# Kernel optimization log

Measured on AMD Instinct MI355X. Metric: run time of the kernel, lower is better.

Reference implementation:

```python
import jax, jax.numpy as jnp
import numpy as np

jax.config.update("jax_enable_x64", True)

MANT_SCALE = 8388608.0  # 2**23


def _decode_fp32_bits(bits):
    """[..., 32] {0,1} pulses (MSB-first IEEE-754 float32) -> float64 value."""
    f64 = jnp.float64
    sign = 1.0 - 2.0 * bits[..., 0].astype(f64)
    e = jnp.einsum('...j,j->...', bits[..., 1:9].astype(f64),
                   jnp.exp2(jnp.arange(7, -1, -1, dtype=f64)))
    frac = jnp.einsum('...j,j->...', bits[..., 9:32].astype(f64),
                      jnp.exp2(-jnp.arange(1, 24, dtype=f64)))
    normal = sign * jnp.exp2(e - 127.0) * (1.0 + frac)
    subnorm = sign * jnp.exp2(-126.0) * frac
    return jnp.where(e > 0, normal, subnorm)


def _encode_fp32_bits(y):
    """float64 value already on the fp32 grid -> [..., 32] {0,1} pulses (MSB-first)."""
    f64 = jnp.float64
    sbit = (y < 0).astype(f64)
    a = jnp.abs(y)
    e = jnp.clip(jnp.floor(jnp.log2(jnp.where(a > 0, a, 1.0))), -126.0, 127.0)
    eb = jnp.where(a > 0, e + 127.0, 0.0)          # biased exponent, 0 for zero/subnormal
    frac = jnp.where(eb > 0, a * jnp.exp2(-e) - 1.0, a * jnp.exp2(126.0))
    mant = frac * MANT_SCALE                        # exact integer for fp32-grid y
    ebits = jnp.mod(jnp.floor(eb[..., None] * jnp.exp2(-jnp.arange(7, -1, -1, dtype=f64))), 2.0)
    mbits = jnp.mod(jnp.floor(mant[..., None] * jnp.exp2(-jnp.arange(22, -1, -1, dtype=f64))), 2.0)
    bits = jnp.concatenate([sbit[..., None], ebits, mbits], axis=-1)
    return jnp.where((a > 0)[..., None], bits, 0.0).astype(jnp.float32)


def setup_inputs() -> dict:
    rng = np.random.default_rng(0)
    vals = (rng.standard_normal((1, 2048, 1024)) * 2.0).astype(np.float32)
    words = vals.view(np.uint32)
    shifts = np.arange(31, -1, -1, dtype=np.uint32)
    bits = ((words[..., None] >> shifts) & np.uint32(1)).astype(np.float32)
    return {"x": jnp.asarray(bits)}


def reference(x):
    # GELU(x) ~= x * sigmoid(1.702 * x), all intermediates in fp64 (as the
    # gate-level pipeline does), final result rounded once to fp32 bits.
    xv = _decode_fp32_bits(x)
    y64 = xv * jax.nn.sigmoid(1.702 * xv)
    y32 = y64.astype(jnp.float32).astype(jnp.float64)  # FP64 -> FP32 rounding
    return _encode_fp32_bits(y32)
```

## Files before the change

### kernel.cpp

```cpp
#include <hip/hip_runtime.h>
#include <math.h>

__global__ __launch_bounds__(256) void spike_gelu_kernel(
    const uint4* __restrict__ in, uint4* __restrict__ out, int n_vals) {
#pragma clang fp contract(off)
  const double LN2 = 0x1.62e42fefa39efp-1;

  __shared__ double Wdec[8], Vdec[23], Lm[23];
  int tid = threadIdx.x;
  if (tid < 8)       Wdec[tid]      = exp((double)(7 - tid) * LN2);
  else if (tid < 31) Vdec[tid - 8]  = exp((double)(7 - tid) * LN2);
  else if (tid < 54) Lm[tid - 31]   = exp((double)(31 - tid) * LN2);
  __syncthreads();

  int v = blockIdx.x * blockDim.x + tid;
  if (v >= n_vals) return;

  const uint4* p = in + (size_t)v * 8;
  uint32_t w = 0;
#pragma unroll
  for (int j = 0; j < 8; ++j) {
    uint4 b = p[j];
    w = (w << 4) | (((b.x >> 23) & 1u) << 3) | (((b.y >> 23) & 1u) << 2) |
        (((b.z >> 23) & 1u) << 1) | ((b.w >> 23) & 1u);
  }

  double sign = (w >> 31) ? -1.0 : 1.0;
  double e_c = 0.0;
#pragma unroll
  for (int j = 0; j < 8; ++j)
    if ((w >> (30 - j)) & 1u) e_c = e_c + Wdec[j];
  double frac_d = 0.0;
#pragma unroll
  for (int j = 0; j < 23; ++j)
    if ((w >> (22 - j)) & 1u) frac_d = frac_d + Vdec[j];

  double x;
  if (e_c > 0.0) {
    double E1 = exp((e_c - 127.0) * LN2);
    x = (sign * E1) * (1.0 + frac_d);
  } else {
    x = (sign * exp(-126.0 * LN2)) * frac_d;
  }

  double t = 1.702 * x;
  double s = 1.0 / (1.0 + exp(-t));
  double y = x * s;
  float yf = (float)y;
  double yd = (double)yf;

  double a = fabs(yd);
  uint32_t ob = 0;
  if (a > 0.0) {
    if (yd < 0.0) ob |= 0x80000000u;
    double e0 = floor(log(a) / LN2);
    e0 = fmin(fmax(e0, -126.0), 127.0);
    double eb = e0 + 127.0;
    double p2 = exp(-e0 * LN2);
    double m1 = a * p2;
    double frac_e = m1 - 1.0;
    double mant = frac_e * 8388608.0;
#pragma unroll
    for (int sc = 7; sc >= 0; --sc) {
      double f = floor(eb * Lm[sc]);
      double md = f - 2.0 * floor(0.5 * f);
      ob |= ((uint32_t)md) << (23 + sc);
    }
#pragma unroll
    for (int sc = 22; sc >= 0; --sc) {
      double f = floor(mant * Lm[sc]);
      double md = f - 2.0 * floor(0.5 * f);
      ob |= ((uint32_t)md) << sc;
    }
  }

  uint4* q = out + (size_t)v * 8;
#pragma unroll
  for (int j = 0; j < 8; ++j) {
    int base = 31 - 4 * j;
    uint4 o;
    o.x = ((ob >> base) & 1u) * 0x3F800000u;
    o.y = ((ob >> (base - 1)) & 1u) * 0x3F800000u;
    o.z = ((ob >> (base - 2)) & 1u) * 0x3F800000u;
    o.w = ((ob >> (base - 3)) & 1u) * 0x3F800000u;
    q[j] = o;
  }
}

extern "C" void kernel_launch(void* const* d_in, const int* in_sizes, int n_in,
                              void* d_out, int out_size, void* d_ws, size_t ws_size,
                              hipStream_t stream) {
  int n_vals = in_sizes[0] / 32;
  const int block = 256;
  int grid = (n_vals + block - 1) / block;
  spike_gelu_kernel<<<grid, block, 0, stream>>>(
      (const uint4*)d_in[0], (uint4*)d_out, n_vals);
}
```

Baseline: 484.8 us.

## Coalesce bit-pulse loads and stores via wave shuffles and LDS staging

Each thread now loads consecutive 16-byte chunks so global reads are fully coalesced across the wave, assembling 32-bit words from nibbles with xor shuffles and staging them in shared memory. After computing, results are written back to shared memory and expanded into coalesced uint4 stores. This replaces the per-thread strided 128-byte access pattern, at the cost of two block barriers and extra LDS traffic.

```diff
diff --git a/kernel.cpp b/kernel.cpp
--- a/kernel.cpp
+++ b/kernel.cpp
@@ -7,83 +7,103 @@
   const double LN2 = 0x1.62e42fefa39efp-1;
 
   __shared__ double Wdec[8], Vdec[23], Lm[23];
-  int tid = threadIdx.x;
+  __shared__ uint32_t lds_w[256];
+
+  const int tid = threadIdx.x;
   if (tid < 8)       Wdec[tid]      = exp((double)(7 - tid) * LN2);
   else if (tid < 31) Vdec[tid - 8]  = exp((double)(7 - tid) * LN2);
   else if (tid < 54) Lm[tid - 31]   = exp((double)(31 - tid) * LN2);
+
+  const int n_chunks = n_vals * 8;
+  const int blk_chunk0 = blockIdx.x * 2048;
+
+  const int nibshift = 28 - 4 * (tid & 7);
+#pragma unroll
+  for (int i = 0; i < 8; ++i) {
+    int g = blk_chunk0 + i * 256 + tid;
+    uint32_t nib = 0;
+    if (g < n_chunks) {
+      uint4 b = in[g];
+      nib = (((b.x >> 23) & 1u) << 3) | (((b.y >> 23) & 1u) << 2) |
+            (((b.z >> 23) & 1u) << 1) | ((b.w >> 23) & 1u);
+    }
+    uint32_t part = nib << nibshift;
+    part |= __shfl_xor(part, 1);
+    part |= __shfl_xor(part, 2);
+    part |= __shfl_xor(part, 4);
+    if ((tid & 7) == 0) lds_w[i * 32 + (tid >> 3)] = part;
+  }
   __syncthreads();
 
-  int v = blockIdx.x * blockDim.x + tid;
-  if (v >= n_vals) return;
+  const int v = blockIdx.x * 256 + tid;
+  uint32_t ob = 0;
+  if (v < n_vals) {
+    const uint32_t w = lds_w[tid];
 
-  const uint4* p = in + (size_t)v * 8;
-  uint32_t w = 0;
+    double sign = (w >> 31) ? -1.0 : 1.0;
+    double e_c = 0.0;
 #pragma unroll
-  for (int j = 0; j < 8; ++j) {
-    uint4 b = p[j];
-    w = (w << 4) | (((b.x >> 23) & 1u) << 3) | (((b.y >> 23) & 1u) << 2) |
-        (((b.z >> 23) & 1u) << 1) | ((b.w >> 23) & 1u);
-  }
+    for (int j = 0; j < 8; ++j)
+      if ((w >> (30 - j)) & 1u) e_c = e_c + Wdec[j];
+    double frac_d = 0.0;
+#pragma unroll
+    for (int j = 0; j < 23; ++j)
+      if ((w >> (22 - j)) & 1u) frac_d = frac_d + Vdec[j];
 
-  double sign = (w >> 31) ? -1.0 : 1.0;
-  double e_c = 0.0;
+    double x;
+    if (e_c > 0.0) {
+      double E1 = exp((e_c - 127.0) * LN2);
+      x = (sign * E1) * (1.0 + frac_d);
+    } else {
+      x = (sign * exp(-126.0 * LN2)) * frac_d;
+    }
+
+    double t = 1.702 * x;
+    double s = 1.0 / (1.0 + exp(-t));
+    double y = x * s;
+    float yf = (float)y;
+    double yd = (double)yf;
+
+    double a = fabs(yd);
+    if (a > 0.0) {
+      if (yd < 0.0) ob |= 0x80000000u;
+      double e0 = floor(log(a) / LN2);
+      e0 = fmin(fmax(e0, -126.0), 127.0);
+      double eb = e0 + 127.0;
+      double p2 = exp(-e0 * LN2);
+      double m1 = a * p2;
+      double frac_e = m1 - 1.0;
+      double mant = frac_e * 8388608.0;
 #pragma unroll
-  for (int j = 0; j < 8; ++j)
-    if ((w >> (30 - j)) & 1u) e_c = e_c + Wdec[j];
-  double frac_d = 0.0;
+      for (int sc = 7; sc >= 0; --sc) {
+        double f = floor(eb * Lm[sc]);
+        double md = f - 2.0 * floor(0.5 * f);
+        ob |= ((uint32_t)md) << (23 + sc);
+      }
 #pragma unroll
-  for (int j = 0; j < 23; ++j)
-    if ((w >> (22 - j)) & 1u) frac_d = frac_d + Vdec[j];
-
-  double x;
-  if (e_c > 0.0) {
-    double E1 = exp((e_c - 127.0) * LN2);
-    x = (sign * E1) * (1.0 + frac_d);
-  } else {
-    x = (sign * exp(-126.0 * LN2)) * frac_d;
-  }
-
-  double t = 1.702 * x;
-  double s = 1.0 / (1.0 + exp(-t));
-  double y = x * s;
-  float yf = (float)y;
-  double yd = (double)yf;
-
-  double a = fabs(yd);
-  uint32_t ob = 0;
-  if (a > 0.0) {
-    if (yd < 0.0) ob |= 0x80000000u;
-    double e0 = floor(log(a) / LN2);
-    e0 = fmin(fmax(e0, -126.0), 127.0);
-    double eb = e0 + 127.0;
-    double p2 = exp(-e0 * LN2);
-    double m1 = a * p2;
-    double frac_e = m1 - 1.0;
-    double mant = frac_e * 8388608.0;
-#pragma unroll
-    for (int sc = 7; sc >= 0; --sc) {
-      double f = floor(eb * Lm[sc]);
-      double md = f - 2.0 * floor(0.5 * f);
-      ob |= ((uint32_t)md) << (23 + sc);
-    }
-#pragma unroll
-    for (int sc = 22; sc >= 0; --sc) {
-      double f = floor(mant * Lm[sc]);
-      double md = f - 2.0 * floor(0.5 * f);
-      ob |= ((uint32_t)md) << sc;
+      for (int sc = 22; sc >= 0; --sc) {
+        double f = floor(mant * Lm[sc]);
+        double md = f - 2.0 * floor(0.5 * f);
+        ob |= ((uint32_t)md) << sc;
+      }
     }
   }
+  lds_w[tid] = ob;
+  __syncthreads();
 
-  uint4* q = out + (size_t)v * 8;
 #pragma unroll
-  for (int j = 0; j < 8; ++j) {
-    int base = 31 - 4 * j;
-    uint4 o;
-    o.x = ((ob >> base) & 1u) * 0x3F800000u;
-    o.y = ((ob >> (base - 1)) & 1u) * 0x3F800000u;
-    o.z = ((ob >> (base - 2)) & 1u) * 0x3F800000u;
-    o.w = ((ob >> (base - 3)) & 1u) * 0x3F800000u;
-    q[j] = o;
+  for (int i = 0; i < 8; ++i) {
+    int g = blk_chunk0 + i * 256 + tid;
+    if (g < n_chunks) {
+      uint32_t wv = lds_w[i * 32 + (tid >> 3)];
+      int base = 31 - 4 * (tid & 7);
+      uint4 o;
+      o.x = ((wv >> base) & 1u) * 0x3F800000u;
+      o.y = ((wv >> (base - 1)) & 1u) * 0x3F800000u;
+      o.z = ((wv >> (base - 2)) & 1u) * 0x3F800000u;
+      o.w = ((wv >> (base - 3)) & 1u) * 0x3F800000u;
+      out[g] = o;
+    }
   }
 }
 
```

Measured after the change: 437.6 us. -9.7%, faster.
